# Kernel optimization log

Hardware: AMD Instinct MI355X
Metric: run time of the kernel (lower is better)

Reference implementation:

```python
import jax, jax.numpy as jnp
import numpy as np

LN_EPS = 1e-5
NORM_EPS = 1e-12
SLOPE = 0.1

def _layernorm(x, g, b):
    m = jnp.mean(x, axis=-1, keepdims=True)
    v = jnp.mean(jnp.square(x - m), axis=-1, keepdims=True)
    return (x - m) * jax.lax.rsqrt(v + LN_EPS) * g + b

def _leaky(x):
    return jnp.where(x >= 0, x, SLOPE * x)

def setup_inputs() -> dict:
    key = jax.random.key(0)
    ks = jax.random.split(key, 8)
    N = 1048576
    features = jax.random.normal(ks[0], (N, 128), dtype=jnp.float32)
    # PyTorch Linear default init: U(-1/sqrt(fan_in), 1/sqrt(fan_in))
    W1 = jax.random.uniform(ks[1], (32, 128), jnp.float32, -1/np.sqrt(128), 1/np.sqrt(128))
    g1 = jnp.ones((32,), jnp.float32); b1 = jnp.zeros((32,), jnp.float32)
    W2 = jax.random.uniform(ks[2], (16, 32), jnp.float32, -1/np.sqrt(32), 1/np.sqrt(32))
    g2 = jnp.ones((16,), jnp.float32); b2 = jnp.zeros((16,), jnp.float32)
    W3 = jax.random.uniform(ks[3], (3, 16), jnp.float32, -1/np.sqrt(16), 1/np.sqrt(16))
    b3 = jax.random.uniform(ks[4], (3,), jnp.float32, -1/np.sqrt(16), 1/np.sqrt(16))
    return {"features": features, "W1": W1, "g1": g1, "b1": b1,
            "W2": W2, "g2": g2, "b2": b2, "W3": W3, "b3": b3}

def reference(features, W1, g1, b1, W2, g2, b2, W3, b3):
    x = features @ W1.T                       # [N,32]
    x = _leaky(_layernorm(x, g1, b1))
    x = x @ W2.T                               # [N,16]
    x = _leaky(_layernorm(x, g2, b2))
    x = x @ W3.T + b3                          # [N,3]
    # F.normalize(dim=-1): x / max(||x||_2, eps)
    n = jnp.linalg.norm(x, axis=-1, keepdims=True)
    return x / jnp.maximum(n, NORM_EPS)
```

## Files before the change

kernel.cpp:

```cpp
#include <hip/hip_runtime.h>
#include <math.h>

typedef short bf16x8 __attribute__((ext_vector_type(8)));
typedef float f32x4  __attribute__((ext_vector_type(4)));

#define TPB 256
#define ROWS 256
#define CSTRIDE 36
#define BFR_BYTES 16384
#define CT_BYTES (ROWS * CSTRIDE * 4)
#define PK(lo, hi) (((lo) >> 16) | ((hi) & 0xffff0000u))
#define BOFF(nt, ks, p) ((((nt)*4 + (ks))*2 + (p))*256)
#define GRID 768

#define WBAR() do { asm volatile("s_waitcnt lgkmcnt(0)" ::: "memory"); \
                    __builtin_amdgcn_s_barrier(); } while (0)

__device__ __forceinline__ void split2A(float x, unsigned &h1, unsigned &h2) {
    unsigned u = __float_as_uint(x);
    h1 = (u + 0x7fffu + ((u >> 16) & 1u)) & 0xffff0000u;
    h2 = __float_as_uint(x - __uint_as_float(h1));
}
__device__ __forceinline__ void split2W(float x, unsigned &h1, unsigned &h2) {
    unsigned u = __float_as_uint(x);
    h1 = (u + 0x7fffu + ((u >> 16) & 1u)) & 0xffff0000u;
    float r1 = x - __uint_as_float(h1);
    unsigned u1 = __float_as_uint(r1);
    h2 = (u1 + 0x7fffu + ((u1 >> 16) & 1u)) & 0xffff0000u;
}

__global__ __launch_bounds__(TPB, 3) void decoder_kernel(
    const float* __restrict__ feat,
    const float* __restrict__ W1, const float* __restrict__ g1, const float* __restrict__ b1,
    const float* __restrict__ W2, const float* __restrict__ g2, const float* __restrict__ b2,
    const float* __restrict__ W3, const float* __restrict__ b3,
    float* __restrict__ out, int N,
    unsigned* __restrict__ ctr, unsigned nchunks)
{
    __shared__ __align__(16) unsigned char lds[BFR_BYTES + CT_BYTES + 16];
    unsigned* bfr = (unsigned*)lds;
    float*    Ct  = (float*)(lds + BFR_BYTES);
    volatile unsigned* nxt_sh = (volatile unsigned*)(lds + BFR_BYTES + CT_BYTES);

    const int t = threadIdx.x;
    const int l = t & 63;
    const int w = t >> 6;
    const int arow = l & 15;
    const int acol = (l >> 4) * 8;

    for (int c = t; c < 512; c += 256) {
        const int lc = c & 63, ks = (c >> 6) & 3, nt = (c >> 8) & 1;
        const float* wp = W1 + (nt * 16 + (lc & 15)) * 128 + ks * 32 + (lc >> 4) * 8;
        float v[8];
        *(float4*)(v)     = *(const float4*)(wp);
        *(float4*)(v + 4) = *(const float4*)(wp + 4);
        unsigned h1[8], h2[8];
#pragma unroll
        for (int i = 0; i < 8; ++i) split2W(v[i], h1[i], h2[i]);
        uint4 q1 = {PK(h1[0],h1[1]), PK(h1[2],h1[3]), PK(h1[4],h1[5]), PK(h1[6],h1[7])};
        uint4 q2 = {PK(h2[0],h2[1]), PK(h2[2],h2[3]), PK(h2[4],h2[5]), PK(h2[6],h2[7])};
        *(uint4*)(bfr + BOFF(nt, ks, 0) + lc * 4) = q1;
        *(uint4*)(bfr + BOFF(nt, ks, 1) + lc * 4) = q2;
    }
    if (t == 0) *nxt_sh = atomicAdd(ctr, 1u);
    __syncthreads();
    unsigned cur = *nxt_sh;

    float4 buf[2][8];
    if (cur < nchunks) {
        size_t rr = (size_t)cur * ROWS + (size_t)w * 64 + arow;
        if (rr >= (size_t)N) rr = N - 1;
        const float* ap = feat + rr * 128 + acol;
#pragma unroll
        for (int ks = 0; ks < 4; ++ks) {
            buf[0][2 * ks]     = *(const float4*)(ap + ks * 32);
            buf[0][2 * ks + 1] = *(const float4*)(ap + ks * 32 + 4);
        }
    }

    while (cur < nchunks) {
        const size_t blk0 = (size_t)cur * ROWS;

#pragma unroll
        for (int j = 0; j < 4; ++j) {
            if (j == 1 && t == 0) *nxt_sh = atomicAdd(ctr, 1u);
            if (j < 3) {
                size_t rr = blk0 + (size_t)w * 64 + (j + 1) * 16 + arow;
                if (rr >= (size_t)N) rr = N - 1;
                const float* ap = feat + rr * 128 + acol;
#pragma unroll
                for (int ks = 0; ks < 4; ++ks) {
                    buf[(j + 1) & 1][2 * ks]     = *(const float4*)(ap + ks * 32);
                    buf[(j + 1) & 1][2 * ks + 1] = *(const float4*)(ap + ks * 32 + 4);
                }
            }
            f32x4 acc0 = {0.f, 0.f, 0.f, 0.f};
            f32x4 acc1 = {0.f, 0.f, 0.f, 0.f};
#pragma unroll
            for (int ks = 0; ks < 4; ++ks) {
                float v[8];
                *(float4*)(v)     = buf[j & 1][2 * ks];
                *(float4*)(v + 4) = buf[j & 1][2 * ks + 1];
                unsigned h1[8], h2[8];
#pragma unroll
                for (int i = 0; i < 8; ++i) split2A(v[i], h1[i], h2[i]);
                uint4 q1 = {PK(h1[0],h1[1]), PK(h1[2],h1[3]), PK(h1[4],h1[5]), PK(h1[6],h1[7])};
                uint4 q2 = {PK(h2[0],h2[1]), PK(h2[2],h2[3]), PK(h2[4],h2[5]), PK(h2[6],h2[7])};
                bf16x8 a1 = __builtin_bit_cast(bf16x8, q1);
                bf16x8 a2 = __builtin_bit_cast(bf16x8, q2);
                bf16x8 B10 = __builtin_bit_cast(bf16x8, *(const uint4*)(bfr + BOFF(0, ks, 0) + l * 4));
                bf16x8 B20 = __builtin_bit_cast(bf16x8, *(const uint4*)(bfr + BOFF(0, ks, 1) + l * 4));
                bf16x8 B11 = __builtin_bit_cast(bf16x8, *(const uint4*)(bfr + BOFF(1, ks, 0) + l * 4));
                bf16x8 B21 = __builtin_bit_cast(bf16x8, *(const uint4*)(bfr + BOFF(1, ks, 1) + l * 4));
                acc0 = __builtin_amdgcn_mfma_f32_16x16x32_bf16(a1, B10, acc0, 0, 0, 0);
                acc1 = __builtin_amdgcn_mfma_f32_16x16x32_bf16(a1, B11, acc1, 0, 0, 0);
                acc0 = __builtin_amdgcn_mfma_f32_16x16x32_bf16(a2, B10, acc0, 0, 0, 0);
                acc1 = __builtin_amdgcn_mfma_f32_16x16x32_bf16(a2, B11, acc1, 0, 0, 0);
                acc0 = __builtin_amdgcn_mfma_f32_16x16x32_bf16(a1, B20, acc0, 0, 0, 0);
                acc1 = __builtin_amdgcn_mfma_f32_16x16x32_bf16(a1, B21, acc1, 0, 0, 0);
            }
            const int crow = w * 64 + j * 16 + (l >> 4) * 4;
            const int ccol = l & 15;
#pragma unroll
            for (int r = 0; r < 4; ++r) {
                Ct[(crow + r) * CSTRIDE + ccol]      = acc0[r];
                Ct[(crow + r) * CSTRIDE + 16 + ccol] = acc1[r];
            }
        }
        WBAR();

        float x[32];
#pragma unroll
        for (int c = 0; c < 8; ++c)
            *(float4*)(x + c * 4) = *(const float4*)(Ct + t * CSTRIDE + c * 4);
        const unsigned nxt = *nxt_sh;
        WBAR();

        if (nxt < nchunks) {
            size_t rr = (size_t)nxt * ROWS + (size_t)w * 64 + arow;
            if (rr >= (size_t)N) rr = N - 1;
            const float* ap = feat + rr * 128 + acol;
#pragma unroll
            for (int ks = 0; ks < 4; ++ks) {
                buf[0][2 * ks]     = *(const float4*)(ap + ks * 32);
                buf[0][2 * ks + 1] = *(const float4*)(ap + ks * 32 + 4);
            }
        }

        float m = 0.f;
#pragma unroll
        for (int j = 0; j < 32; ++j) m += x[j];
        m *= (1.f / 32.f);
        float var = 0.f;
#pragma unroll
        for (int j = 0; j < 32; ++j) { const float d = x[j] - m; var = fmaf(d, d, var); }
        var *= (1.f / 32.f);
        const float rs1 = rsqrtf(var + 1e-5f);

        float z[32];
#pragma unroll
        for (int j = 0; j < 32; ++j) {
            float y = (x[j] - m) * rs1 * g1[j] + b1[j];
            z[j] = (y >= 0.f) ? y : 0.1f * y;
        }

        float a2v[16];
#pragma unroll
        for (int k = 0; k < 16; ++k) {
            const float* __restrict__ wrow = W2 + k * 32;
            float s = 0.f;
#pragma unroll
            for (int j = 0; j < 32; ++j) s = fmaf(z[j], wrow[j], s);
            a2v[k] = s;
        }

        float m2 = 0.f;
#pragma unroll
        for (int k = 0; k < 16; ++k) m2 += a2v[k];
        m2 *= (1.f / 16.f);
        float v2 = 0.f;
#pragma unroll
        for (int k = 0; k < 16; ++k) { const float d = a2v[k] - m2; v2 = fmaf(d, d, v2); }
        v2 *= (1.f / 16.f);
        const float rs2 = rsqrtf(v2 + 1e-5f);

        float z2[16];
#pragma unroll
        for (int k = 0; k < 16; ++k) {
            float y = (a2v[k] - m2) * rs2 * g2[k] + b2[k];
            z2[k] = (y >= 0.f) ? y : 0.1f * y;
        }

        float o[3];
#pragma unroll
        for (int q = 0; q < 3; ++q) {
            const float* __restrict__ wrow = W3 + q * 16;
            float s = b3[q];
#pragma unroll
            for (int k = 0; k < 16; ++k) s = fmaf(z2[k], wrow[k], s);
            o[q] = s;
        }
        const float nrm = sqrtf(o[0]*o[0] + o[1]*o[1] + o[2]*o[2]);
        const float inv = 1.f / fmaxf(nrm, 1e-12f);

        const size_t myrow = blk0 + t;
        if (myrow < (size_t)N) {
            out[myrow * 3 + 0] = o[0] * inv;
            out[myrow * 3 + 1] = o[1] * inv;
            out[myrow * 3 + 2] = o[2] * inv;
        }

        cur = nxt;
    }
}

extern "C" void kernel_launch(void* const* d_in, const int* in_sizes, int n_in,
                              void* d_out, int out_size, void* d_ws, size_t ws_size,
                              hipStream_t stream) {
    const float* feat = (const float*)d_in[0];
    const float* W1   = (const float*)d_in[1];
    const float* g1   = (const float*)d_in[2];
    const float* b1   = (const float*)d_in[3];
    const float* W2   = (const float*)d_in[4];
    const float* g2   = (const float*)d_in[5];
    const float* b2   = (const float*)d_in[6];
    const float* W3   = (const float*)d_in[7];
    const float* b3   = (const float*)d_in[8];
    float* out = (float*)d_out;

    const int N = in_sizes[0] / 128;
    const unsigned nchunks = (unsigned)((N + ROWS - 1) / ROWS);
    unsigned* ctr = (unsigned*)d_ws;

    hipMemsetAsync(ctr, 0, sizeof(unsigned), stream);
    decoder_kernel<<<GRID, TPB, 0, stream>>>(feat, W1, g1, b1, W2, g2, b2, W3, b3,
                                             out, N, ctr, nchunks);
}
```

Baseline: 126.5 us.

## Make each wavefront fetch its own 64-row chunk and drop block barriers

Work distribution changes from per-block 256-row chunks to per-wavefront 64-row chunks. Each wave claims a chunk with its own atomic, broadcasts the result via readfirstlane, and uses a private slice of LDS for the C tile, so both workgroup barriers go away. The prefetch of the next chunk's first tile now happens inside the last MFMA iteration rather than after the barrier. The cost is four times as many atomics on one global counter, and correctness of the LDS handoff relies on intra-wave ordering with no explicit wait.

```diff
diff --git a/kernel.cpp b/kernel.cpp
--- a/kernel.cpp
+++ b/kernel.cpp
@@ -5,16 +5,13 @@
 typedef float f32x4  __attribute__((ext_vector_type(4)));
 
 #define TPB 256
-#define ROWS 256
+#define WROWS 64
 #define CSTRIDE 36
 #define BFR_BYTES 16384
-#define CT_BYTES (ROWS * CSTRIDE * 4)
+#define CT_BYTES (256 * CSTRIDE * 4)
 #define PK(lo, hi) (((lo) >> 16) | ((hi) & 0xffff0000u))
 #define BOFF(nt, ks, p) ((((nt)*4 + (ks))*2 + (p))*256)
 #define GRID 768
-
-#define WBAR() do { asm volatile("s_waitcnt lgkmcnt(0)" ::: "memory"); \
-                    __builtin_amdgcn_s_barrier(); } while (0)
 
 __device__ __forceinline__ void split2A(float x, unsigned &h1, unsigned &h2) {
     unsigned u = __float_as_uint(x);
@@ -37,16 +34,15 @@
     float* __restrict__ out, int N,
     unsigned* __restrict__ ctr, unsigned nchunks)
 {
-    __shared__ __align__(16) unsigned char lds[BFR_BYTES + CT_BYTES + 16];
+    __shared__ __align__(16) unsigned char lds[BFR_BYTES + CT_BYTES];
     unsigned* bfr = (unsigned*)lds;
-    float*    Ct  = (float*)(lds + BFR_BYTES);
-    volatile unsigned* nxt_sh = (volatile unsigned*)(lds + BFR_BYTES + CT_BYTES);
 
     const int t = threadIdx.x;
     const int l = t & 63;
     const int w = t >> 6;
     const int arow = l & 15;
     const int acol = (l >> 4) * 8;
+    float* myCt = (float*)(lds + BFR_BYTES) + w * WROWS * CSTRIDE;
 
     for (int c = t; c < 512; c += 256) {
         const int lc = c & 63, ks = (c >> 6) & 3, nt = (c >> 8) & 1;
@@ -62,13 +58,15 @@
         *(uint4*)(bfr + BOFF(nt, ks, 0) + lc * 4) = q1;
         *(uint4*)(bfr + BOFF(nt, ks, 1) + lc * 4) = q2;
     }
-    if (t == 0) *nxt_sh = atomicAdd(ctr, 1u);
     __syncthreads();
-    unsigned cur = *nxt_sh;
+
+    unsigned v0 = 0;
+    if (l == 0) v0 = atomicAdd(ctr, 1u);
+    unsigned cur = (unsigned)__builtin_amdgcn_readfirstlane((int)v0);
 
     float4 buf[2][8];
     if (cur < nchunks) {
-        size_t rr = (size_t)cur * ROWS + (size_t)w * 64 + arow;
+        size_t rr = (size_t)cur * WROWS + arow;
         if (rr >= (size_t)N) rr = N - 1;
         const float* ap = feat + rr * 128 + acol;
 #pragma unroll
@@ -79,13 +77,19 @@
     }
 
     while (cur < nchunks) {
-        const size_t blk0 = (size_t)cur * ROWS;
+        const size_t blk0 = (size_t)cur * WROWS;
+
+        unsigned v1 = 0;
+        if (l == 0) v1 = atomicAdd(ctr, 1u);
+        const unsigned nxt = (unsigned)__builtin_amdgcn_readfirstlane((int)v1);
 
 #pragma unroll
         for (int j = 0; j < 4; ++j) {
-            if (j == 1 && t == 0) *nxt_sh = atomicAdd(ctr, 1u);
-            if (j < 3) {
-                size_t rr = blk0 + (size_t)w * 64 + (j + 1) * 16 + arow;
+            const bool pf_valid = (j < 3) | (nxt < nchunks);
+            if (pf_valid) {
+                const size_t pbase = (j < 3) ? (blk0 + (j + 1) * 16)
+                                             : ((size_t)nxt * WROWS);
+                size_t rr = pbase + arow;
                 if (rr >= (size_t)N) rr = N - 1;
                 const float* ap = feat + rr * 128 + acol;
 #pragma unroll
@@ -119,33 +123,19 @@
                 acc0 = __builtin_amdgcn_mfma_f32_16x16x32_bf16(a1, B20, acc0, 0, 0, 0);
                 acc1 = __builtin_amdgcn_mfma_f32_16x16x32_bf16(a1, B21, acc1, 0, 0, 0);
             }
-            const int crow = w * 64 + j * 16 + (l >> 4) * 4;
+            const int crow = j * 16 + (l >> 4) * 4;
             const int ccol = l & 15;
 #pragma unroll
             for (int r = 0; r < 4; ++r) {
-                Ct[(crow + r) * CSTRIDE + ccol]      = acc0[r];
-                Ct[(crow + r) * CSTRIDE + 16 + ccol] = acc1[r];
+                myCt[(crow + r) * CSTRIDE + ccol]      = acc0[r];
+                myCt[(crow + r) * CSTRIDE + 16 + ccol] = acc1[r];
             }
         }
-        WBAR();
 
         float x[32];
 #pragma unroll
         for (int c = 0; c < 8; ++c)
-            *(float4*)(x + c * 4) = *(const float4*)(Ct + t * CSTRIDE + c * 4);
-        const unsigned nxt = *nxt_sh;
-        WBAR();
-
-        if (nxt < nchunks) {
-            size_t rr = (size_t)nxt * ROWS + (size_t)w * 64 + arow;
-            if (rr >= (size_t)N) rr = N - 1;
-            const float* ap = feat + rr * 128 + acol;
-#pragma unroll
-            for (int ks = 0; ks < 4; ++ks) {
-                buf[0][2 * ks]     = *(const float4*)(ap + ks * 32);
-                buf[0][2 * ks + 1] = *(const float4*)(ap + ks * 32 + 4);
-            }
-        }
+            *(float4*)(x + c * 4) = *(const float4*)(myCt + l * CSTRIDE + c * 4);
 
         float m = 0.f;
 #pragma unroll
@@ -203,7 +193,7 @@
         const float nrm = sqrtf(o[0]*o[0] + o[1]*o[1] + o[2]*o[2]);
         const float inv = 1.f / fmaxf(nrm, 1e-12f);
 
-        const size_t myrow = blk0 + t;
+        const size_t myrow = blk0 + l;
         if (myrow < (size_t)N) {
             out[myrow * 3 + 0] = o[0] * inv;
             out[myrow * 3 + 1] = o[1] * inv;
@@ -229,7 +219,7 @@
     float* out = (float*)d_out;
 
     const int N = in_sizes[0] / 128;
-    const unsigned nchunks = (unsigned)((N + ROWS - 1) / ROWS);
+    const unsigned nchunks = (unsigned)((N + WROWS - 1) / WROWS);
     unsigned* ctr = (unsigned*)d_ws;
 
     hipMemsetAsync(ctr, 0, sizeof(unsigned), stream);
```

Measured after the change: 281.4 us. +122.5%, slower.
